# Performance work log

Hardware: AMD Instinct MI355X
Metric: run time of the kernel (lower is better)

Reference implementation:

```python
import jax, jax.numpy as jnp
import numpy as np

NUM_NODES = 100000
EMBED_DIM = 64
NUM_LAYERS = 3
NUM_EDGES = 3200000


def setup_inputs() -> dict:
    key = jax.random.key(0)
    k1, k2 = jax.random.split(key)
    # xavier_uniform for [N, D]: bound = sqrt(6/(N+D))
    bound = float(np.sqrt(6.0 / (NUM_NODES + EMBED_DIM)))
    emb = jax.random.uniform(k1, (NUM_NODES, EMBED_DIM), dtype=jnp.float32,
                             minval=-bound, maxval=bound)
    edge_index = jax.random.randint(k2, (2, NUM_EDGES), 0, NUM_NODES, dtype=jnp.int64)
    return {"emb": emb, "edge_index": edge_index}


def reference(emb, edge_index):
    # LightGCN: xs = [x0, LGConv(x0), LGConv^2(x0), ...]; output = mean(xs)
    # LGConv (PyG, add_self_loops=False): out[i] = sum_{(j,i) in E} x[j] / sqrt(d_j * d_i)
    n = emb.shape[0]
    row, col = edge_index[0], edge_index[1]  # row = source j, col = target i
    ones = jnp.ones(row.shape[0], dtype=emb.dtype)
    deg = jax.ops.segment_sum(ones, col, num_segments=n)  # in-degree per gcn_norm
    dinv = jnp.where(deg > 0, jax.lax.rsqrt(jnp.where(deg > 0, deg, 1.0)), 0.0)
    norm = dinv[row] * dinv[col]  # [E]

    x = emb
    acc = emb
    for _ in range(NUM_LAYERS):
        msgs = x[row] * norm[:, None]                      # gather + normalize [E, D]
        x = jax.ops.segment_sum(msgs, col, num_segments=n)  # scatter-add [N, D]
        acc = acc + x
    return acc / (NUM_LAYERS + 1)
```

## Files before the change

kernel.cpp:

```cpp
#include <hip/hip_runtime.h>
#include <hip/hip_bf16.h>
#include <hip/hip_fp16.h>
#include <stdint.h>


#define N_NODES 100000
#define N_EDGES 3200000
#define DIM 64

#define BSH 7
#define BNODES 128
#define NB 782
#define CAP 4608

#define CHUNK 4096
#define NBLK1 ((N_EDGES + CHUNK - 1) / CHUNK)

__global__ __launch_bounds__(256) void k_bucket(const int* __restrict__ ei,
                                                int* __restrict__ gcursor,
                                                int* __restrict__ staging) {
    __shared__ int stage[CHUNK];
    __shared__ unsigned short sbkt[CHUNK];
    __shared__ int bcnt[NB];
    __shared__ int boff[NB];
    __shared__ int bstart[NB];
    __shared__ int gbase[NB];
    __shared__ int wtt[4];

    int t = threadIdx.x;
    int e0 = blockIdx.x * CHUNK;
    int nblk = min(CHUNK, N_EDGES - e0);
    int nvec = nblk >> 2;

    const int4* col4 = (const int4*)(ei + N_EDGES + e0);
    const int4* row4 = (const int4*)(ei + e0);

    for (int i = t; i < NB; i += 256) { bcnt[i] = 0; boff[i] = 0; }
    __syncthreads();

    for (int i = t; i < nvec; i += 256) {
        int4 c = col4[i];
        atomicAdd(&bcnt[c.x >> BSH], 1);
        atomicAdd(&bcnt[c.y >> BSH], 1);
        atomicAdd(&bcnt[c.z >> BSH], 1);
        atomicAdd(&bcnt[c.w >> BSH], 1);
    }
    __syncthreads();

    {
        int v[4];
        int s = 0;
#pragma unroll
        for (int k = 0; k < 4; k++) {
            int j = t * 4 + k;
            v[k] = (j < NB) ? bcnt[j] : 0;
            s += v[k];
        }
        int lane = t & 63, w = t >> 6;
        int ss = s;
#pragma unroll
        for (int off = 1; off < 64; off <<= 1) {
            int u = __shfl_up(ss, off);
            if (lane >= off) ss += u;
        }
        if (lane == 63) wtt[w] = ss;
        __syncthreads();
        int wo = 0;
        for (int ww = 0; ww < w; ww++) wo += wtt[ww];
        int run = ss - s + wo;
#pragma unroll
        for (int k = 0; k < 4; k++) {
            int j = t * 4 + k;
            if (j < NB) {
                bstart[j] = run;
                gbase[j] = (v[k] > 0) ? atomicAdd(&gcursor[j], v[k]) : 0;
            }
            run += v[k];
        }
    }
    __syncthreads();

    for (int i = t; i < nvec; i += 256) {
        int4 c = col4[i];
        int4 r = row4[i];
        int b0 = c.x >> BSH, b1 = c.y >> BSH, b2 = c.z >> BSH, b3 = c.w >> BSH;
        int p0 = bstart[b0] + atomicAdd(&boff[b0], 1);
        int p1 = bstart[b1] + atomicAdd(&boff[b1], 1);
        int p2 = bstart[b2] + atomicAdd(&boff[b2], 1);
        int p3 = bstart[b3] + atomicAdd(&boff[b3], 1);
        stage[p0] = (r.x << BSH) | (c.x & (BNODES - 1)); sbkt[p0] = (unsigned short)b0;
        stage[p1] = (r.y << BSH) | (c.y & (BNODES - 1)); sbkt[p1] = (unsigned short)b1;
        stage[p2] = (r.z << BSH) | (c.z & (BNODES - 1)); sbkt[p2] = (unsigned short)b2;
        stage[p3] = (r.w << BSH) | (c.w & (BNODES - 1)); sbkt[p3] = (unsigned short)b3;
    }
    __syncthreads();

    for (int i = t; i < nblk; i += 256) {
        int e = stage[i];
        int b = sbkt[i];
        staging[(size_t)b * CAP + gbase[b] + (i - bstart[b])] = e;
    }
}

__global__ void k_bstart(const int* __restrict__ gcursor, int* __restrict__ bucketStart) {
    __shared__ int wtt[4];
    int t = threadIdx.x;
    int v[4];
    int s = 0;
#pragma unroll
    for (int k = 0; k < 4; k++) {
        int j = t * 4 + k;
        v[k] = (j < NB) ? gcursor[j] : 0;
        s += v[k];
    }
    int lane = t & 63, w = t >> 6;
    int ss = s;
#pragma unroll
    for (int off = 1; off < 64; off <<= 1) {
        int u = __shfl_up(ss, off);
        if (lane >= off) ss += u;
    }
    if (lane == 63) wtt[w] = ss;
    __syncthreads();
    int wo = 0;
    for (int ww = 0; ww < w; ww++) wo += wtt[ww];
    int run = ss - s + wo;
#pragma unroll
    for (int k = 0; k < 4; k++) {
        int j = t * 4 + k;
        if (j < NB) bucketStart[j] = run;
        run += v[k];
    }
}

__global__ __launch_bounds__(256) void k_build(const int* __restrict__ gcursor,
                                               const int* __restrict__ bucketStart,
                                               const int* __restrict__ staging,
                                               int4* __restrict__ rec,
                                               float* __restrict__ dinv,
                                               int* __restrict__ csrc) {
    __shared__ int ldeg[BNODES];
    __shared__ int lcur[BNODES];
    __shared__ int wtt[4];

    int b = blockIdx.x;
    int t = threadIdx.x;
    int n0 = b << BSH;
    int nloc = min(BNODES, N_NODES - n0);
    int cnt = gcursor[b];
    const int* st = staging + (size_t)b * CAP;

    if (t < BNODES) ldeg[t] = 0;
    __syncthreads();

    for (int i = t; i < cnt; i += 256) {
        atomicAdd(&ldeg[st[i] & (BNODES - 1)], 1);
    }
    __syncthreads();

    int a = (t < BNODES) ? ldeg[t] : 0;
    int lane = t & 63, w = t >> 6;
    int ss = a;
#pragma unroll
    for (int off = 1; off < 64; off <<= 1) {
        int u = __shfl_up(ss, off);
        if (lane >= off) ss += u;
    }
    if (lane == 63) wtt[w] = ss;
    __syncthreads();
    int wo = 0;
    for (int ww = 0; ww < w; ww++) wo += wtt[ww];
    int excl = ss - a + wo;
    int gb = bucketStart[b] + excl;

    if (t < BNODES) {
        lcur[t] = gb;
        if (t < nloc) {
            int n = n0 + t;
            float di = (a > 0) ? rsqrtf((float)a) : 0.0f;
            rec[n] = make_int4(gb, a, __float_as_int(di), 0);
            dinv[n] = di;
        }
    }
    __syncthreads();

    for (int i = t; i < cnt; i += 256) {
        int e = st[i];
        int p = atomicAdd(&lcur[e & (BNODES - 1)], 1);
        csrc[p] = e >> BSH;
    }
}

__global__ void k_z0(const float* __restrict__ emb, const float* __restrict__ dinv,
                     __half* __restrict__ zA, __half* __restrict__ zB) {
    const int total = (N_NODES * DIM) / 4;
    int i = blockIdx.x * blockDim.x + threadIdx.x;
    if (i >= total) {
        int r = i - total;
        if (r < 16) ((uint2*)(zA + (size_t)N_NODES * DIM))[r] = make_uint2(0, 0);
        else if (r < 32) ((uint2*)(zB + (size_t)N_NODES * DIM))[r - 16] = make_uint2(0, 0);
        return;
    }
    float di = dinv[(i * 4) >> 6];
    const float4 v = ((const float4*)emb)[i];
    union { ushort h[4]; uint2 u; } pk;
    __half h0 = __float2half(v.x * di);
    __half h1 = __float2half(v.y * di);
    __half h2 = __float2half(v.z * di);
    __half h3 = __float2half(v.w * di);
    pk.h[0] = *(ushort*)&h0; pk.h[1] = *(ushort*)&h1;
    pk.h[2] = *(ushort*)&h2; pk.h[3] = *(ushort*)&h3;
    ((uint2*)zA)[i] = pk.u;
}

__global__ __launch_bounds__(256) void k_spmv(
    const int4* __restrict__ rec, const int* __restrict__ csrc,
    const __half* __restrict__ z, __half* __restrict__ znext,
    const __half* __restrict__ zprev, const float* __restrict__ emb,
    float* __restrict__ out, int mode) {
    int wave = (blockIdx.x * blockDim.x + threadIdx.x) >> 6;
    int lane = threadIdx.x & 63;
    if (wave >= N_NODES) return;
    int g = lane >> 3;
    int l = lane & 7;

    int4 nr = rec[wave];
    int start = nr.x;
    int cnt = nr.y;
    float di = __int_as_float(nr.z);
    int ng = (cnt + 7) >> 3;

    __half2 hz = __float2half2_rn(0.0f);
    __half2 hacc0 = hz, hacc1 = hz, hacc2 = hz, hacc3 = hz;

#define GLOAD(KK, SVAR)                              \
    int e##SVAR = (KK) * 8 + g;                      \
    int SVAR = csrc[start + e##SVAR];                \
    SVAR = (e##SVAR < cnt) ? SVAR : N_NODES;

#define GACC(SVAR)                                                        \
    do {                                                                  \
        uint4 v = *((const uint4*)(z + ((size_t)SVAR << 6)) + l);         \
        const __half2* hv = (const __half2*)&v;                           \
        hacc0 = __hadd2(hacc0, hv[0]);                                    \
        hacc1 = __hadd2(hacc1, hv[1]);                                    \
        hacc2 = __hadd2(hacc2, hv[2]);                                    \
        hacc3 = __hadd2(hacc3, hv[3]);                                    \
    } while (0)

    int k = 0;
    for (; k + 4 <= ng; k += 4) {
        GLOAD(k + 0, s0); GLOAD(k + 1, s1); GLOAD(k + 2, s2); GLOAD(k + 3, s3);
        GACC(s0); GACC(s1); GACC(s2); GACC(s3);
    }
    int rem = ng - k;
    if (rem > 0) {
        GLOAD(k + 0, t0);
        if (rem > 1) { GLOAD(k + 1, t1);
            if (rem > 2) { GLOAD(k + 2, t2); GACC(t0); GACC(t1); GACC(t2); }
            else { GACC(t0); GACC(t1); }
        } else { GACC(t0); }
    }
#undef GLOAD
#undef GACC

#pragma unroll
    for (int off = 8; off <= 32; off <<= 1) {
        int b0 = __shfl_xor(*(int*)&hacc0, off);
        int b1 = __shfl_xor(*(int*)&hacc1, off);
        int b2 = __shfl_xor(*(int*)&hacc2, off);
        int b3 = __shfl_xor(*(int*)&hacc3, off);
        hacc0 = __hadd2(hacc0, *(__half2*)&b0);
        hacc1 = __hadd2(hacc1, *(__half2*)&b1);
        hacc2 = __hadd2(hacc2, *(__half2*)&b2);
        hacc3 = __hadd2(hacc3, *(__half2*)&b3);
    }

    if (lane < 8) {
        size_t o = (size_t)wave * DIM + lane * 8;
        float x[8];
        x[0] = __low2float(hacc0) * di; x[1] = __high2float(hacc0) * di;
        x[2] = __low2float(hacc1) * di; x[3] = __high2float(hacc1) * di;
        x[4] = __low2float(hacc2) * di; x[5] = __high2float(hacc2) * di;
        x[6] = __low2float(hacc3) * di; x[7] = __high2float(hacc3) * di;

        if (mode == 0) {
            union { ushort h[8]; uint4 u; } pk;
#pragma unroll
            for (int j = 0; j < 8; j++) {
                __half hh = __float2half(x[j] * di);
                pk.h[j] = *(ushort*)&hh;
            }
            *((uint4*)(znext + o)) = pk.u;
        } else {
            float sdeg = (cnt > 0) ? sqrtf((float)cnt) : 0.0f;
            uint4 v2 = *((const uint4*)(zprev + o));
            uint4 v3 = *((const uint4*)(z + o));
            const __half2* h2 = (const __half2*)&v2;
            const __half2* h3 = (const __half2*)&v3;
            float4 e0 = ((const float4*)(emb + o))[0];
            float4 e1 = ((const float4*)(emb + o))[1];
            float zs[8];
#pragma unroll
            for (int j = 0; j < 4; j++) {
                float2 a2 = __half22float2(h2[j]);
                float2 a3 = __half22float2(h3[j]);
                zs[2 * j] = a2.x + a3.x;
                zs[2 * j + 1] = a2.y + a3.y;
            }
            float4 o0 = make_float4(
                (e0.x + sdeg * zs[0] + x[0]) * 0.25f,
                (e0.y + sdeg * zs[1] + x[1]) * 0.25f,
                (e0.z + sdeg * zs[2] + x[2]) * 0.25f,
                (e0.w + sdeg * zs[3] + x[3]) * 0.25f);
            float4 o1 = make_float4(
                (e1.x + sdeg * zs[4] + x[4]) * 0.25f,
                (e1.y + sdeg * zs[5] + x[5]) * 0.25f,
                (e1.z + sdeg * zs[6] + x[6]) * 0.25f,
                (e1.w + sdeg * zs[7] + x[7]) * 0.25f);
            ((float4*)(out + o))[0] = o0;
            ((float4*)(out + o))[1] = o1;
        }
    }
}

extern "C" void kernel_launch(void* const* d_in, const int* in_sizes, int n_in,
                              void* d_out, int out_size, void* d_ws, size_t ws_size,
                              hipStream_t stream) {
    const float* emb = (const float*)d_in[0];
    const int* ei = (const int*)d_in[1];
    float* out = (float*)d_out;

    char* ws = (char*)d_ws;
    size_t off = 0;
    auto alloc = [&](size_t bytes) -> void* {
        void* p = ws + off;
        off += (bytes + 511) & ~(size_t)511;
        return p;
    };
    int4* rec = (int4*)alloc((size_t)N_NODES * 16);
    float* dinv = (float*)alloc((size_t)N_NODES * 4);
    int* gcursor = (int*)alloc(NB * 4);
    int* bucketStart = (int*)alloc(NB * 4);
    int* csrc = (int*)alloc(((size_t)N_EDGES + 64) * 4);
    size_t zbytes = (size_t)(N_NODES + 1) * DIM * 2;
    size_t stbytes = (size_t)NB * CAP * 4;
    char* transient = (char*)alloc(stbytes > zbytes ? stbytes : zbytes);
    int* staging = (int*)transient;
    __half* zA = (__half*)transient;
    __half* zB = (__half*)alloc(zbytes);

    hipMemsetAsync(gcursor, 0, NB * 4, stream);

    k_bucket<<<NBLK1, 256, 0, stream>>>(ei, gcursor, staging);
    k_bstart<<<1, 256, 0, stream>>>(gcursor, bucketStart);
    k_build<<<NB, 256, 0, stream>>>(gcursor, bucketStart, staging, rec, dinv, csrc);
    k_z0<<<(N_NODES * DIM / 4) / 256 + 1, 256, 0, stream>>>(emb, dinv, zA, zB);

    int spmvBlocks = (N_NODES + 3) / 4;
    k_spmv<<<spmvBlocks, 256, 0, stream>>>(rec, csrc, zA, zB, nullptr, emb, out, 0);
    k_spmv<<<spmvBlocks, 256, 0, stream>>>(rec, csrc, zB, zA, nullptr, emb, out, 0);
    k_spmv<<<spmvBlocks, 256, 0, stream>>>(rec, csrc, zA, nullptr, zB, emb, out, 2);
}
```

Before: 337.0 us.

## Use coarser 512-node buckets, fold bucket-start scan into build kernel

Bucket width grows from 128 to 512 destination nodes (196 buckets, 8192-edge chunks), which cuts global cursor atomics and makes staging writes per chunk larger and more contiguous. The separate single-block bucket-start scan kernel is removed; each build block rescans the bucket counts itself. Each bucket is now handled by four build blocks that each own a 128-node quarter, so every block reads the whole bucket and repeats the degree count, and only its own quarter's edges are written. This trades redundant staging reads and degree counting for fewer launches and less atomic contention.

```diff
diff --git a/kernel.cpp b/kernel.cpp
--- a/kernel.cpp
+++ b/kernel.cpp
@@ -8,24 +8,24 @@
 #define N_EDGES 3200000
 #define DIM 64
 
-#define BSH 7
-#define BNODES 128
-#define NB 782
-#define CAP 4608
-
-#define CHUNK 4096
+#define BSH 9
+#define BNODES 512
+#define NB 196
+#define CAP 20480
+
+#define CHUNK 8192
 #define NBLK1 ((N_EDGES + CHUNK - 1) / CHUNK)
 
 __global__ __launch_bounds__(256) void k_bucket(const int* __restrict__ ei,
                                                 int* __restrict__ gcursor,
                                                 int* __restrict__ staging) {
     __shared__ int stage[CHUNK];
-    __shared__ unsigned short sbkt[CHUNK];
+    __shared__ unsigned char sbkt[CHUNK];
     __shared__ int bcnt[NB];
     __shared__ int boff[NB];
     __shared__ int bstart[NB];
     __shared__ int gbase[NB];
-    __shared__ int wtt[4];
+    __shared__ int wt[4];
 
     int t = threadIdx.x;
     int e0 = blockIdx.x * CHUNK;
@@ -48,34 +48,21 @@
     __syncthreads();
 
     {
-        int v[4];
-        int s = 0;
-#pragma unroll
-        for (int k = 0; k < 4; k++) {
-            int j = t * 4 + k;
-            v[k] = (j < NB) ? bcnt[j] : 0;
-            s += v[k];
-        }
+        int v = (t < NB) ? bcnt[t] : 0;
         int lane = t & 63, w = t >> 6;
-        int ss = s;
+        int s = v;
 #pragma unroll
         for (int off = 1; off < 64; off <<= 1) {
-            int u = __shfl_up(ss, off);
-            if (lane >= off) ss += u;
-        }
-        if (lane == 63) wtt[w] = ss;
+            int u = __shfl_up(s, off);
+            if (lane >= off) s += u;
+        }
+        if (lane == 63) wt[w] = s;
         __syncthreads();
         int wo = 0;
-        for (int ww = 0; ww < w; ww++) wo += wtt[ww];
-        int run = ss - s + wo;
-#pragma unroll
-        for (int k = 0; k < 4; k++) {
-            int j = t * 4 + k;
-            if (j < NB) {
-                bstart[j] = run;
-                gbase[j] = (v[k] > 0) ? atomicAdd(&gcursor[j], v[k]) : 0;
-            }
-            run += v[k];
+        for (int ww = 0; ww < w; ww++) wo += wt[ww];
+        if (t < NB) {
+            bstart[t] = s - v + wo;
+            gbase[t] = (v > 0) ? atomicAdd(&gcursor[t], v) : 0;
         }
     }
     __syncthreads();
@@ -88,10 +75,10 @@
         int p1 = bstart[b1] + atomicAdd(&boff[b1], 1);
         int p2 = bstart[b2] + atomicAdd(&boff[b2], 1);
         int p3 = bstart[b3] + atomicAdd(&boff[b3], 1);
-        stage[p0] = (r.x << BSH) | (c.x & (BNODES - 1)); sbkt[p0] = (unsigned short)b0;
-        stage[p1] = (r.y << BSH) | (c.y & (BNODES - 1)); sbkt[p1] = (unsigned short)b1;
-        stage[p2] = (r.z << BSH) | (c.z & (BNODES - 1)); sbkt[p2] = (unsigned short)b2;
-        stage[p3] = (r.w << BSH) | (c.w & (BNODES - 1)); sbkt[p3] = (unsigned short)b3;
+        stage[p0] = (r.x << BSH) | (c.x & (BNODES - 1)); sbkt[p0] = (unsigned char)b0;
+        stage[p1] = (r.y << BSH) | (c.y & (BNODES - 1)); sbkt[p1] = (unsigned char)b1;
+        stage[p2] = (r.z << BSH) | (c.z & (BNODES - 1)); sbkt[p2] = (unsigned char)b2;
+        stage[p3] = (r.w << BSH) | (c.w & (BNODES - 1)); sbkt[p3] = (unsigned char)b3;
     }
     __syncthreads();
 
@@ -102,65 +89,52 @@
     }
 }
 
-__global__ void k_bstart(const int* __restrict__ gcursor, int* __restrict__ bucketStart) {
-    __shared__ int wtt[4];
-    int t = threadIdx.x;
-    int v[4];
-    int s = 0;
-#pragma unroll
-    for (int k = 0; k < 4; k++) {
-        int j = t * 4 + k;
-        v[k] = (j < NB) ? gcursor[j] : 0;
-        s += v[k];
-    }
-    int lane = t & 63, w = t >> 6;
-    int ss = s;
-#pragma unroll
-    for (int off = 1; off < 64; off <<= 1) {
-        int u = __shfl_up(ss, off);
-        if (lane >= off) ss += u;
-    }
-    if (lane == 63) wtt[w] = ss;
-    __syncthreads();
-    int wo = 0;
-    for (int ww = 0; ww < w; ww++) wo += wtt[ww];
-    int run = ss - s + wo;
-#pragma unroll
-    for (int k = 0; k < 4; k++) {
-        int j = t * 4 + k;
-        if (j < NB) bucketStart[j] = run;
-        run += v[k];
-    }
-}
-
 __global__ __launch_bounds__(256) void k_build(const int* __restrict__ gcursor,
-                                               const int* __restrict__ bucketStart,
                                                const int* __restrict__ staging,
                                                int4* __restrict__ rec,
                                                float* __restrict__ dinv,
                                                int* __restrict__ csrc) {
     __shared__ int ldeg[BNODES];
     __shared__ int lcur[BNODES];
+    __shared__ int gsc[NB];
     __shared__ int wtt[4];
 
-    int b = blockIdx.x;
+    int b = blockIdx.x >> 2;
+    int q = blockIdx.x & 3;
     int t = threadIdx.x;
     int n0 = b << BSH;
     int nloc = min(BNODES, N_NODES - n0);
     int cnt = gcursor[b];
     const int* st = staging + (size_t)b * CAP;
 
-    if (t < BNODES) ldeg[t] = 0;
-    __syncthreads();
+    {
+        int v = (t < NB) ? gcursor[t] : 0;
+        int lane = t & 63, w = t >> 6;
+        int ss = v;
+#pragma unroll
+        for (int off = 1; off < 64; off <<= 1) {
+            int u = __shfl_up(ss, off);
+            if (lane >= off) ss += u;
+        }
+        if (lane == 63) wtt[w] = ss;
+        ldeg[t] = 0; ldeg[t + 256] = 0;
+        __syncthreads();
+        int wo = 0;
+        for (int ww = 0; ww < w; ww++) wo += wtt[ww];
+        if (t < NB) gsc[t] = ss - v + wo;
+    }
+    __syncthreads();
+    int bstartB = gsc[b];
 
     for (int i = t; i < cnt; i += 256) {
         atomicAdd(&ldeg[st[i] & (BNODES - 1)], 1);
     }
     __syncthreads();
 
-    int a = (t < BNODES) ? ldeg[t] : 0;
+    int a0 = ldeg[2 * t], a1 = ldeg[2 * t + 1];
+    int s = a0 + a1;
     int lane = t & 63, w = t >> 6;
-    int ss = a;
+    int ss = s;
 #pragma unroll
     for (int off = 1; off < 64; off <<= 1) {
         int u = __shfl_up(ss, off);
@@ -170,24 +144,33 @@
     __syncthreads();
     int wo = 0;
     for (int ww = 0; ww < w; ww++) wo += wtt[ww];
-    int excl = ss - a + wo;
-    int gb = bucketStart[b] + excl;
-
-    if (t < BNODES) {
-        lcur[t] = gb;
-        if (t < nloc) {
-            int n = n0 + t;
-            float di = (a > 0) ? rsqrtf((float)a) : 0.0f;
-            rec[n] = make_int4(gb, a, __float_as_int(di), 0);
+    int excl = ss - s + wo;
+
+    int gb = bstartB + excl;
+    int n = n0 + 2 * t;
+    lcur[2 * t] = gb;
+    lcur[2 * t + 1] = gb + a0;
+    if (((2 * t) >> 7) == q) {
+        if (2 * t < nloc) {
+            float di = (a0 > 0) ? rsqrtf((float)a0) : 0.0f;
+            rec[n] = make_int4(gb, a0, __float_as_int(di), 0);
             dinv[n] = di;
+        }
+        if (2 * t + 1 < nloc) {
+            float di = (a1 > 0) ? rsqrtf((float)a1) : 0.0f;
+            rec[n + 1] = make_int4(gb + a0, a1, __float_as_int(di), 0);
+            dinv[n + 1] = di;
         }
     }
     __syncthreads();
 
     for (int i = t; i < cnt; i += 256) {
         int e = st[i];
-        int p = atomicAdd(&lcur[e & (BNODES - 1)], 1);
-        csrc[p] = e >> BSH;
+        int dl = e & (BNODES - 1);
+        if ((dl >> 7) == q) {
+            int p = atomicAdd(&lcur[dl], 1);
+            csrc[p] = e >> BSH;
+        }
     }
 }
 
@@ -341,7 +324,6 @@
     int4* rec = (int4*)alloc((size_t)N_NODES * 16);
     float* dinv = (float*)alloc((size_t)N_NODES * 4);
     int* gcursor = (int*)alloc(NB * 4);
-    int* bucketStart = (int*)alloc(NB * 4);
     int* csrc = (int*)alloc(((size_t)N_EDGES + 64) * 4);
     size_t zbytes = (size_t)(N_NODES + 1) * DIM * 2;
     size_t stbytes = (size_t)NB * CAP * 4;
@@ -353,8 +335,7 @@
     hipMemsetAsync(gcursor, 0, NB * 4, stream);
 
     k_bucket<<<NBLK1, 256, 0, stream>>>(ei, gcursor, staging);
-    k_bstart<<<1, 256, 0, stream>>>(gcursor, bucketStart);
-    k_build<<<NB, 256, 0, stream>>>(gcursor, bucketStart, staging, rec, dinv, csrc);
+    k_build<<<NB * 4, 256, 0, stream>>>(gcursor, staging, rec, dinv, csrc);
     k_z0<<<(N_NODES * DIM / 4) / 256 + 1, 256, 0, stream>>>(emb, dinv, zA, zB);
 
     int spmvBlocks = (N_NODES + 3) / 4;
```

Measured after the change: 307.9 us. -8.6%, faster.

## Fold bucket-start scan into build kernel, halve chunk size, batch SpMV gathers

Applied to the files above, without the earlier changes.

Removes the separate single-block prefix-scan launch by having each build block recompute the exclusive scan of bucket counts itself. The bucketing chunk size drops from 4096 to 2048 edges, which gives more blocks and less shared memory per block. The SpMV gather is reorganized so that nodes with at most 64 in-edges issue all 8 index loads and then all 8 row fetches before accumulating, exposing more memory-level parallelism. The costs are redundant scan work in every build block and more global atomics on gcursor from the extra bucket blocks.

```diff
diff --git a/kernel.cpp b/kernel.cpp
--- a/kernel.cpp
+++ b/kernel.cpp
@@ -8,12 +8,13 @@
 #define N_EDGES 3200000
 #define DIM 64
 
-#define BSH 7
-#define BNODES 128
-#define NB 782
-#define CAP 4608
-
-#define CHUNK 4096
+#define QSH 7
+#define QNODES 128
+#define NBQ 782
+#define NBQP 784
+#define CAP_Q 4608
+
+#define CHUNK 2048
 #define NBLK1 ((N_EDGES + CHUNK - 1) / CHUNK)
 
 __global__ __launch_bounds__(256) void k_bucket(const int* __restrict__ ei,
@@ -21,11 +22,11 @@
                                                 int* __restrict__ staging) {
     __shared__ int stage[CHUNK];
     __shared__ unsigned short sbkt[CHUNK];
-    __shared__ int bcnt[NB];
-    __shared__ int boff[NB];
-    __shared__ int bstart[NB];
-    __shared__ int gbase[NB];
-    __shared__ int wtt[4];
+    __shared__ int bcnt[NBQP];
+    __shared__ int boff[NBQP];
+    __shared__ int bstart[NBQP];
+    __shared__ int gbase[NBQP];
+    __shared__ int wt[4];
 
     int t = threadIdx.x;
     int e0 = blockIdx.x * CHUNK;
@@ -35,15 +36,15 @@
     const int4* col4 = (const int4*)(ei + N_EDGES + e0);
     const int4* row4 = (const int4*)(ei + e0);
 
-    for (int i = t; i < NB; i += 256) { bcnt[i] = 0; boff[i] = 0; }
+    for (int i = t; i < NBQP; i += 256) { bcnt[i] = 0; boff[i] = 0; }
     __syncthreads();
 
     for (int i = t; i < nvec; i += 256) {
         int4 c = col4[i];
-        atomicAdd(&bcnt[c.x >> BSH], 1);
-        atomicAdd(&bcnt[c.y >> BSH], 1);
-        atomicAdd(&bcnt[c.z >> BSH], 1);
-        atomicAdd(&bcnt[c.w >> BSH], 1);
+        atomicAdd(&bcnt[c.x >> QSH], 1);
+        atomicAdd(&bcnt[c.y >> QSH], 1);
+        atomicAdd(&bcnt[c.z >> QSH], 1);
+        atomicAdd(&bcnt[c.w >> QSH], 1);
     }
     __syncthreads();
 
@@ -53,7 +54,7 @@
 #pragma unroll
         for (int k = 0; k < 4; k++) {
             int j = t * 4 + k;
-            v[k] = (j < NB) ? bcnt[j] : 0;
+            v[k] = (j < NBQ) ? bcnt[j] : 0;
             s += v[k];
         }
         int lane = t & 63, w = t >> 6;
@@ -63,7 +64,79 @@
             int u = __shfl_up(ss, off);
             if (lane >= off) ss += u;
         }
+        if (lane == 63) wt[w] = ss;
+        __syncthreads();
+        int wo = 0;
+        for (int ww = 0; ww < w; ww++) wo += wt[ww];
+        int run = ss - s + wo;
+#pragma unroll
+        for (int k = 0; k < 4; k++) {
+            int j = t * 4 + k;
+            if (j < NBQ) {
+                bstart[j] = run;
+                gbase[j] = (v[k] > 0) ? atomicAdd(&gcursor[j], v[k]) : 0;
+            }
+            run += v[k];
+        }
+    }
+    __syncthreads();
+
+    for (int i = t; i < nvec; i += 256) {
+        int4 c = col4[i];
+        int4 r = row4[i];
+        int b0 = c.x >> QSH, b1 = c.y >> QSH, b2 = c.z >> QSH, b3 = c.w >> QSH;
+        int p0 = bstart[b0] + atomicAdd(&boff[b0], 1);
+        int p1 = bstart[b1] + atomicAdd(&boff[b1], 1);
+        int p2 = bstart[b2] + atomicAdd(&boff[b2], 1);
+        int p3 = bstart[b3] + atomicAdd(&boff[b3], 1);
+        stage[p0] = (r.x << QSH) | (c.x & (QNODES - 1)); sbkt[p0] = (unsigned short)b0;
+        stage[p1] = (r.y << QSH) | (c.y & (QNODES - 1)); sbkt[p1] = (unsigned short)b1;
+        stage[p2] = (r.z << QSH) | (c.z & (QNODES - 1)); sbkt[p2] = (unsigned short)b2;
+        stage[p3] = (r.w << QSH) | (c.w & (QNODES - 1)); sbkt[p3] = (unsigned short)b3;
+    }
+    __syncthreads();
+
+    for (int i = t; i < nblk; i += 256) {
+        int e = stage[i];
+        int b = sbkt[i];
+        staging[(size_t)b * CAP_Q + gbase[b] + (i - bstart[b])] = e;
+    }
+}
+
+__global__ __launch_bounds__(256) void k_build(const int* __restrict__ gcursor,
+                                               const int* __restrict__ staging,
+                                               int4* __restrict__ rec,
+                                               float* __restrict__ dinv,
+                                               int* __restrict__ csrc) {
+    __shared__ int ldeg[QNODES];
+    __shared__ int lcur[QNODES];
+    __shared__ int gsc[NBQ];
+    __shared__ int wtt[4];
+
+    int q = blockIdx.x;
+    int t = threadIdx.x;
+    int n0 = q << QSH;
+    int cnt = gcursor[q];
+    const int* st = staging + (size_t)q * CAP_Q;
+
+    {
+        int v[4];
+        int s = 0;
+#pragma unroll
+        for (int k = 0; k < 4; k++) {
+            int j = t * 4 + k;
+            v[k] = (j < NBQ) ? gcursor[j] : 0;
+            s += v[k];
+        }
+        int lane = t & 63, w = t >> 6;
+        int ss = s;
+#pragma unroll
+        for (int off = 1; off < 64; off <<= 1) {
+            int u = __shfl_up(ss, off);
+            if (lane >= off) ss += u;
+        }
         if (lane == 63) wtt[w] = ss;
+        if (t < QNODES) ldeg[t] = 0;
         __syncthreads();
         int wo = 0;
         for (int ww = 0; ww < w; ww++) wo += wtt[ww];
@@ -71,50 +144,21 @@
 #pragma unroll
         for (int k = 0; k < 4; k++) {
             int j = t * 4 + k;
-            if (j < NB) {
-                bstart[j] = run;
-                gbase[j] = (v[k] > 0) ? atomicAdd(&gcursor[j], v[k]) : 0;
-            }
+            if (j < NBQ) gsc[j] = run;
             run += v[k];
         }
     }
     __syncthreads();
-
-    for (int i = t; i < nvec; i += 256) {
-        int4 c = col4[i];
-        int4 r = row4[i];
-        int b0 = c.x >> BSH, b1 = c.y >> BSH, b2 = c.z >> BSH, b3 = c.w >> BSH;
-        int p0 = bstart[b0] + atomicAdd(&boff[b0], 1);
-        int p1 = bstart[b1] + atomicAdd(&boff[b1], 1);
-        int p2 = bstart[b2] + atomicAdd(&boff[b2], 1);
-        int p3 = bstart[b3] + atomicAdd(&boff[b3], 1);
-        stage[p0] = (r.x << BSH) | (c.x & (BNODES - 1)); sbkt[p0] = (unsigned short)b0;
-        stage[p1] = (r.y << BSH) | (c.y & (BNODES - 1)); sbkt[p1] = (unsigned short)b1;
-        stage[p2] = (r.z << BSH) | (c.z & (BNODES - 1)); sbkt[p2] = (unsigned short)b2;
-        stage[p3] = (r.w << BSH) | (c.w & (BNODES - 1)); sbkt[p3] = (unsigned short)b3;
-    }
-    __syncthreads();
-
-    for (int i = t; i < nblk; i += 256) {
-        int e = stage[i];
-        int b = sbkt[i];
-        staging[(size_t)b * CAP + gbase[b] + (i - bstart[b])] = e;
-    }
-}
-
-__global__ void k_bstart(const int* __restrict__ gcursor, int* __restrict__ bucketStart) {
-    __shared__ int wtt[4];
-    int t = threadIdx.x;
-    int v[4];
-    int s = 0;
-#pragma unroll
-    for (int k = 0; k < 4; k++) {
-        int j = t * 4 + k;
-        v[k] = (j < NB) ? gcursor[j] : 0;
-        s += v[k];
-    }
+    int qstart = gsc[q];
+
+    for (int i = t; i < cnt; i += 256) {
+        atomicAdd(&ldeg[st[i] & (QNODES - 1)], 1);
+    }
+    __syncthreads();
+
+    int a = (t < QNODES) ? ldeg[t] : 0;
     int lane = t & 63, w = t >> 6;
-    int ss = s;
+    int ss = a;
 #pragma unroll
     for (int off = 1; off < 64; off <<= 1) {
         int u = __shfl_up(ss, off);
@@ -124,59 +168,13 @@
     __syncthreads();
     int wo = 0;
     for (int ww = 0; ww < w; ww++) wo += wtt[ww];
-    int run = ss - s + wo;
-#pragma unroll
-    for (int k = 0; k < 4; k++) {
-        int j = t * 4 + k;
-        if (j < NB) bucketStart[j] = run;
-        run += v[k];
-    }
-}
-
-__global__ __launch_bounds__(256) void k_build(const int* __restrict__ gcursor,
-                                               const int* __restrict__ bucketStart,
-                                               const int* __restrict__ staging,
-                                               int4* __restrict__ rec,
-                                               float* __restrict__ dinv,
-                                               int* __restrict__ csrc) {
-    __shared__ int ldeg[BNODES];
-    __shared__ int lcur[BNODES];
-    __shared__ int wtt[4];
-
-    int b = blockIdx.x;
-    int t = threadIdx.x;
-    int n0 = b << BSH;
-    int nloc = min(BNODES, N_NODES - n0);
-    int cnt = gcursor[b];
-    const int* st = staging + (size_t)b * CAP;
-
-    if (t < BNODES) ldeg[t] = 0;
-    __syncthreads();
-
-    for (int i = t; i < cnt; i += 256) {
-        atomicAdd(&ldeg[st[i] & (BNODES - 1)], 1);
-    }
-    __syncthreads();
-
-    int a = (t < BNODES) ? ldeg[t] : 0;
-    int lane = t & 63, w = t >> 6;
-    int ss = a;
-#pragma unroll
-    for (int off = 1; off < 64; off <<= 1) {
-        int u = __shfl_up(ss, off);
-        if (lane >= off) ss += u;
-    }
-    if (lane == 63) wtt[w] = ss;
-    __syncthreads();
-    int wo = 0;
-    for (int ww = 0; ww < w; ww++) wo += wtt[ww];
     int excl = ss - a + wo;
-    int gb = bucketStart[b] + excl;
-
-    if (t < BNODES) {
+
+    if (t < QNODES) {
+        int gb = qstart + excl;
         lcur[t] = gb;
-        if (t < nloc) {
-            int n = n0 + t;
+        int n = n0 + t;
+        if (n < N_NODES) {
             float di = (a > 0) ? rsqrtf((float)a) : 0.0f;
             rec[n] = make_int4(gb, a, __float_as_int(di), 0);
             dinv[n] = di;
@@ -186,8 +184,8 @@
 
     for (int i = t; i < cnt; i += 256) {
         int e = st[i];
-        int p = atomicAdd(&lcur[e & (BNODES - 1)], 1);
-        csrc[p] = e >> BSH;
+        int p = atomicAdd(&lcur[e & (QNODES - 1)], 1);
+        csrc[p] = e >> QSH;
     }
 }
 
@@ -233,36 +231,46 @@
     __half2 hz = __float2half2_rn(0.0f);
     __half2 hacc0 = hz, hacc1 = hz, hacc2 = hz, hacc3 = hz;
 
-#define GLOAD(KK, SVAR)                              \
-    int e##SVAR = (KK) * 8 + g;                      \
-    int SVAR = csrc[start + e##SVAR];                \
-    SVAR = (e##SVAR < cnt) ? SVAR : N_NODES;
-
-#define GACC(SVAR)                                                        \
+#define GIDX(KK, SV)                                 \
+    int e_##SV = (KK) * 8 + g;                       \
+    int SV = csrc[start + e_##SV];                   \
+    SV = (e_##SV < cnt) ? SV : N_NODES;
+
+#define GFETCH(SV, VV)                               \
+    uint4 VV = *((const uint4*)(z + ((size_t)SV << 6)) + l);
+
+#define GADD(VV)                                                          \
     do {                                                                  \
-        uint4 v = *((const uint4*)(z + ((size_t)SVAR << 6)) + l);         \
-        const __half2* hv = (const __half2*)&v;                           \
+        const __half2* hv = (const __half2*)&VV;                          \
         hacc0 = __hadd2(hacc0, hv[0]);                                    \
         hacc1 = __hadd2(hacc1, hv[1]);                                    \
         hacc2 = __hadd2(hacc2, hv[2]);                                    \
         hacc3 = __hadd2(hacc3, hv[3]);                                    \
     } while (0)
 
-    int k = 0;
-    for (; k + 4 <= ng; k += 4) {
-        GLOAD(k + 0, s0); GLOAD(k + 1, s1); GLOAD(k + 2, s2); GLOAD(k + 3, s3);
-        GACC(s0); GACC(s1); GACC(s2); GACC(s3);
-    }
-    int rem = ng - k;
-    if (rem > 0) {
-        GLOAD(k + 0, t0);
-        if (rem > 1) { GLOAD(k + 1, t1);
-            if (rem > 2) { GLOAD(k + 2, t2); GACC(t0); GACC(t1); GACC(t2); }
-            else { GACC(t0); GACC(t1); }
-        } else { GACC(t0); }
-    }
-#undef GLOAD
-#undef GACC
+    if (ng <= 8) {
+        GIDX(0, s0) GIDX(1, s1) GIDX(2, s2) GIDX(3, s3)
+        GIDX(4, s4) GIDX(5, s5) GIDX(6, s6) GIDX(7, s7)
+        GFETCH(s0, v0) GFETCH(s1, v1) GFETCH(s2, v2) GFETCH(s3, v3)
+        GFETCH(s4, v4) GFETCH(s5, v5) GFETCH(s6, v6) GFETCH(s7, v7)
+        GADD(v0); GADD(v1); GADD(v2); GADD(v3);
+        GADD(v4); GADD(v5); GADD(v6); GADD(v7);
+    } else {
+        int k = 0;
+        for (; k + 4 <= ng; k += 4) {
+            GIDX(k + 0, s0) GIDX(k + 1, s1) GIDX(k + 2, s2) GIDX(k + 3, s3)
+            GFETCH(s0, v0) GFETCH(s1, v1) GFETCH(s2, v2) GFETCH(s3, v3)
+            GADD(v0); GADD(v1); GADD(v2); GADD(v3);
+        }
+        for (; k < ng; k++) {
+            GIDX(k, sA)
+            GFETCH(sA, vA)
+            GADD(vA);
+        }
+    }
+#undef GIDX
+#undef GFETCH
+#undef GADD
 
 #pragma unroll
     for (int off = 8; off <= 32; off <<= 1) {
@@ -340,21 +348,19 @@
     };
     int4* rec = (int4*)alloc((size_t)N_NODES * 16);
     float* dinv = (float*)alloc((size_t)N_NODES * 4);
-    int* gcursor = (int*)alloc(NB * 4);
-    int* bucketStart = (int*)alloc(NB * 4);
+    int* gcursor = (int*)alloc(NBQ * 4);
     int* csrc = (int*)alloc(((size_t)N_EDGES + 64) * 4);
     size_t zbytes = (size_t)(N_NODES + 1) * DIM * 2;
-    size_t stbytes = (size_t)NB * CAP * 4;
+    size_t stbytes = (size_t)NBQ * CAP_Q * 4;
     char* transient = (char*)alloc(stbytes > zbytes ? stbytes : zbytes);
     int* staging = (int*)transient;
     __half* zA = (__half*)transient;
     __half* zB = (__half*)alloc(zbytes);
 
-    hipMemsetAsync(gcursor, 0, NB * 4, stream);
+    hipMemsetAsync(gcursor, 0, NBQ * 4, stream);
 
     k_bucket<<<NBLK1, 256, 0, stream>>>(ei, gcursor, staging);
-    k_bstart<<<1, 256, 0, stream>>>(gcursor, bucketStart);
-    k_build<<<NB, 256, 0, stream>>>(gcursor, bucketStart, staging, rec, dinv, csrc);
+    k_build<<<NBQ, 256, 0, stream>>>(gcursor, staging, rec, dinv, csrc);
     k_z0<<<(N_NODES * DIM / 4) / 256 + 1, 256, 0, stream>>>(emb, dinv, zA, zB);
 
     int spmvBlocks = (N_NODES + 3) / 4;
```

New measurement: 395.7 us. 17.4% more time.
